# Kernel tuning notes

Hardware: AMD Instinct MI355X
Metric: run time of the kernel (lower is better)

The kernel has to match this reference:

```python
import jax, jax.numpy as jnp
import numpy as np

DIM = 256
DIM_HEAD = 32
HEADS = DIM // DIM_HEAD
SCALE = DIM_HEAD ** -0.5


def setup_inputs() -> dict:
    key = jax.random.key(0)
    ks = jax.random.split(key, 8)
    D1 = DIM + 1
    s = 1.0 / np.sqrt(D1)
    x = jax.random.normal(ks[0], (2, 32, 32, 8, 8, D1), dtype=jnp.float32)
    Wqv = jax.random.normal(ks[1], (D1, DIM), dtype=jnp.float32) * s
    Wkv = jax.random.normal(ks[2], (D1, DIM), dtype=jnp.float32) * s
    Wvv = jax.random.normal(ks[3], (D1, DIM), dtype=jnp.float32) * s
    Wqd = jax.random.normal(ks[4], (D1, 1), dtype=jnp.float32) * s
    Wkd = jax.random.normal(ks[5], (D1, 1), dtype=jnp.float32) * s
    Wvd = jax.random.normal(ks[6], (D1, 1), dtype=jnp.float32) * s
    Wout = jax.random.normal(ks[7], (D1, D1), dtype=jnp.float32) * s
    return {"x": x, "Wqv": Wqv, "Wkv": Wkv, "Wvv": Wvv,
            "Wqd": Wqd, "Wkd": Wkd, "Wvd": Wvd, "Wout": Wout}


def reference(x, Wqv, Wkv, Wvv, Wqd, Wkd, Wvd, Wout):
    b, gx, gy, w1, w2, D1 = x.shape
    B = b * gx * gy          # number of windows
    n = w1 * w2              # tokens per window
    h, dh = HEADS, DIM_HEAD
    xf = x.reshape(B, n, D1)

    def split_heads(t, nh, d):
        # (B, n, nh*d) -> (B, nh, n, d)
        return t.reshape(B, n, nh, d).transpose(0, 2, 1, 3)

    qv = split_heads(xf @ Wqv, h, dh) * SCALE
    kv = split_heads(xf @ Wkv, h, dh)
    vv = split_heads(xf @ Wvv, h, dh)
    qd = split_heads(xf @ Wqd, 1, 1) * SCALE
    kd = split_heads(xf @ Wkd, 1, 1)
    vd = split_heads(xf @ Wvd, 1, 1)

    sim_v = jnp.einsum('bhid,bhjd->bhij', qv, kv)          # (B, h, n, n)
    sim_d = jnp.einsum('bhid,bhjd->bhij', qd, kd)          # (B, 1, n, n)
    sim_m = sim_v * jax.nn.sigmoid(sim_d)                  # depth-gated scores

    attn_v = jax.nn.softmax(sim_m, axis=-1)                # (B, h, n, n)
    attn_d = jax.nn.softmax(jnp.sum(sim_m, axis=1, keepdims=True), axis=-1)  # (B,1,n,n)

    out_v = jnp.einsum('bhij,bhjd->bhid', attn_v, vv)      # (B, h, n, dh)
    out_d = jnp.einsum('bhij,bhjd->bhid', attn_d, vd)      # (B, 1, n, 1)

    out_v = out_v.transpose(0, 2, 1, 3).reshape(B, n, h * dh)  # (B, n, dim)
    out_d = out_d.transpose(0, 2, 1, 3).reshape(B, n, 1)       # (B, n, 1)

    out = jnp.concatenate([out_v, out_d], axis=-1) @ Wout      # (B, n, dim+1)
    return out.reshape(b, gx, gy, w1, w2, D1)
```

## Files before the change

kernel.cpp:

```cpp
#include <hip/hip_runtime.h>


#define D1    257
#define NTOK  64
#define NH    8
#define KT    9
#define NT_CAT 49
#define NT_OUT 17
#define SCALE 0.17677669529663687f

#define XS_OFF    0
#define XS_STRIDE 296
#define OC_STRIDE 288
#define QS_OFF    37888
#define QK_STRIDE 264
#define KS_OFF    71680
#define VS_OFF    105472
#define VS_STRIDE 72
#define AT_OFF    142336
#define AT_STRIDE 72
#define QD_OFF    151552
#define KD_OFF    151808
#define VD_OFF    152064
#define LDS_SIZE  152320

#define WCAT_ELEMS (KT * NT_CAT * 512)
#define WOUT_ELEMS (KT * NT_OUT * 512)

using bf16x8 = __attribute__((ext_vector_type(8))) short;
using s16x4  = __attribute__((ext_vector_type(4))) short;
using f32x4  = __attribute__((ext_vector_type(4))) float;

__device__ __forceinline__ short f2b(float f) {
  unsigned u = __float_as_uint(f);
  u = (u + 0x7FFFu + ((u >> 16) & 1u)) >> 16;
  return (short)u;
}

__device__ __forceinline__ f32x4 mfma16(bf16x8 a, bf16x8 b, f32x4 c) {
  return __builtin_amdgcn_mfma_f32_16x16x32_bf16(a, b, c, 0, 0, 0);
}

__global__ void prep_weights(const float* __restrict__ Wqv, const float* __restrict__ Wkv,
                             const float* __restrict__ Wvv, const float* __restrict__ Wqd,
                             const float* __restrict__ Wkd, const float* __restrict__ Wvd,
                             const float* __restrict__ Wout,
                             short* __restrict__ wcatp, short* __restrict__ woutp) {
  int idx = blockIdx.x * 256 + threadIdx.x;
  if (idx < WCAT_ELEMS) {
    int j = idx & 7, lane = (idx >> 3) & 63, rest = idx >> 9;
    int nt = rest % NT_CAT, kt = rest / NT_CAT;
    int k = 32 * kt + (lane >> 4) * 8 + j;
    int n = 16 * nt + (lane & 15);
    float v = 0.f;
    if (k < D1) {
      if (n < 256)       v = Wqv[k * 256 + n] * SCALE;
      else if (n < 512)  v = Wkv[k * 256 + (n - 256)];
      else if (n < 768)  v = Wvv[k * 256 + (n - 512)];
      else if (n == 768) v = Wqd[k] * SCALE;
      else if (n == 769) v = Wkd[k];
      else if (n == 770) v = Wvd[k];
    }
    wcatp[idx] = f2b(v);
  } else {
    int i2 = idx - WCAT_ELEMS;
    int j = i2 & 7, lane = (i2 >> 3) & 63, rest = i2 >> 9;
    int nt = rest % NT_OUT, kt = rest / NT_OUT;
    int k = 32 * kt + (lane >> 4) * 8 + j;
    int n = 16 * nt + (lane & 15);
    float v = (k < D1 && n < D1) ? Wout[k * D1 + n] : 0.f;
    woutp[i2] = f2b(v);
  }
}

__global__ __launch_bounds__(256, 1)
void vda_attn(const float* __restrict__ x, const short* __restrict__ wcatp,
              const short* __restrict__ woutp, float* __restrict__ out) {
  extern __shared__ char smem[];
  short* xs  = (short*)(smem + XS_OFF);
  short* qs  = (short*)(smem + QS_OFF);
  short* ks  = (short*)(smem + KS_OFF);
  short* vs  = (short*)(smem + VS_OFF);
  short* at  = (short*)(smem + AT_OFF);
  float* qd_s = (float*)(smem + QD_OFF);
  float* kd_s = (float*)(smem + KD_OFF);
  float* vd_s = (float*)(smem + VD_OFF);
  short* oc = xs;

  const int tid  = threadIdx.x;
  const int lane = tid & 63;
  const int w    = tid >> 6;
  const int m    = lane & 15;
  const int q    = lane >> 4;
  const int q8   = q * 8;
  const int win  = blockIdx.x;

  for (int i = tid; i < 64 * 40; i += 256) {
    int r = i / 40, c = 256 + (i % 40);
    if (c > 256) xs[r * XS_STRIDE + c] = 0;
  }
  {
    const float4* xw4 = (const float4*)(x + (size_t)win * (NTOK * D1));
    for (int it = 0; it < 17; ++it) {
      int f4 = tid + it * 256;
      if (f4 < 4112) {
        float4 v = xw4[f4];
        float vals[4] = {v.x, v.y, v.z, v.w};
        int o0 = f4 * 4;
#pragma unroll
        for (int jj = 0; jj < 4; ++jj) {
          int o = o0 + jj;
          int r = o / D1;
          int c = o - r * D1;
          xs[r * XS_STRIDE + c] = f2b(vals[jj]);
        }
      }
    }
  }
  __syncthreads();

  {
    bf16x8 af[4][KT];
#pragma unroll
    for (int mt = 0; mt < 4; ++mt)
#pragma unroll
      for (int kt = 0; kt < KT; ++kt)
        af[mt][kt] = *(const bf16x8*)&xs[(16 * mt + m) * XS_STRIDE + 32 * kt + q8];

    for (int nt = w; nt < NT_CAT; nt += 4) {
      f32x4 acc[4];
#pragma unroll
      for (int mt = 0; mt < 4; ++mt) acc[mt] = f32x4{0.f, 0.f, 0.f, 0.f};
      const short* wp = wcatp + ((size_t)nt * 64 + lane) * 8;
#pragma unroll
      for (int kt = 0; kt < KT; ++kt) {
        bf16x8 bfr = *(const bf16x8*)(wp + (size_t)kt * (NT_CAT * 512));
#pragma unroll
        for (int mt = 0; mt < 4; ++mt)
          acc[mt] = mfma16(af[mt][kt], bfr, acc[mt]);
      }
      int c = nt * 16 + m;
      if (c < 256) {
#pragma unroll
        for (int mt = 0; mt < 4; ++mt)
#pragma unroll
          for (int r = 0; r < 4; ++r)
            qs[(16 * mt + 4 * q + r) * QK_STRIDE + c] = f2b(acc[mt][r]);
      } else if (c < 512) {
#pragma unroll
        for (int mt = 0; mt < 4; ++mt)
#pragma unroll
          for (int r = 0; r < 4; ++r)
            ks[(16 * mt + 4 * q + r) * QK_STRIDE + (c - 256)] = f2b(acc[mt][r]);
      } else if (c < 768) {
        int d = c - 512;
#pragma unroll
        for (int mt = 0; mt < 4; ++mt) {
          s16x4 pk;
#pragma unroll
          for (int r = 0; r < 4; ++r) pk[r] = f2b(acc[mt][r]);
          *(s16x4*)&vs[d * VS_STRIDE + 16 * mt + 4 * q] = pk;
        }
      } else {
        if (m < 3) {
          float* dst = (m == 0) ? qd_s : (m == 1) ? kd_s : vd_s;
#pragma unroll
          for (int mt = 0; mt < 4; ++mt)
#pragma unroll
            for (int r = 0; r < 4; ++r)
              dst[16 * mt + 4 * q + r] = acc[mt][r];
        }
      }
    }
  }
  __syncthreads();

  {
    int row = 16 * w + m;
#pragma unroll
    for (int i = 0; i < 8; ++i)
      oc[row * OC_STRIDE + 256 + q8 + i] = 0;
  }

  float gate[4][4];
  float ssum[4][4];
  {
    float qd_r[4], kd_c[4];
#pragma unroll
    for (int r = 0; r < 4; ++r) qd_r[r] = qd_s[16 * w + 4 * q + r];
#pragma unroll
    for (int nt = 0; nt < 4; ++nt) kd_c[nt] = kd_s[16 * nt + m];
#pragma unroll
    for (int nt = 0; nt < 4; ++nt)
#pragma unroll
      for (int r = 0; r < 4; ++r) {
        float t = qd_r[r] * kd_c[nt];
        gate[nt][r] = 1.f / (1.f + __expf(-t));
        ssum[nt][r] = 0.f;
      }
  }

  short* atw = at + w * (16 * AT_STRIDE);

  for (int h = 0; h < NH; ++h) {
    bf16x8 aq = *(const bf16x8*)&qs[(16 * w + m) * QK_STRIDE + 32 * h + q8];
    f32x4 sv[4];
#pragma unroll
    for (int nt = 0; nt < 4; ++nt) {
      bf16x8 bk = *(const bf16x8*)&ks[(16 * nt + m) * QK_STRIDE + 32 * h + q8];
      f32x4 z = {0.f, 0.f, 0.f, 0.f};
      sv[nt] = mfma16(aq, bk, z);
    }
    float sm[4][4], mx[4], sum[4];
#pragma unroll
    for (int r = 0; r < 4; ++r) mx[r] = -3.4e38f;
#pragma unroll
    for (int nt = 0; nt < 4; ++nt)
#pragma unroll
      for (int r = 0; r < 4; ++r) {
        float s = sv[nt][r] * gate[nt][r];
        ssum[nt][r] += s;
        sm[nt][r] = s;
        mx[r] = fmaxf(mx[r], s);
      }
#pragma unroll
    for (int r = 0; r < 4; ++r) {
#pragma unroll
      for (int msk = 1; msk < 16; msk <<= 1)
        mx[r] = fmaxf(mx[r], __shfl_xor(mx[r], msk));
      sum[r] = 0.f;
    }
#pragma unroll
    for (int nt = 0; nt < 4; ++nt)
#pragma unroll
      for (int r = 0; r < 4; ++r) {
        float p = __expf(sm[nt][r] - mx[r]);
        sm[nt][r] = p;
        sum[r] += p;
      }
#pragma unroll
    for (int r = 0; r < 4; ++r) {
#pragma unroll
      for (int msk = 1; msk < 16; msk <<= 1)
        sum[r] += __shfl_xor(sum[r], msk);
      sum[r] = 1.f / sum[r];
    }
#pragma unroll
    for (int nt = 0; nt < 4; ++nt)
#pragma unroll
      for (int r = 0; r < 4; ++r)
        atw[(4 * q + r) * AT_STRIDE + 16 * nt + m] = f2b(sm[nt][r] * sum[r]);

    bf16x8 a0 = *(const bf16x8*)&atw[m * AT_STRIDE + q8];
    bf16x8 a1 = *(const bf16x8*)&atw[m * AT_STRIDE + 32 + q8];
#pragma unroll
    for (int ntp = 0; ntp < 2; ++ntp) {
      int drow = 32 * h + 16 * ntp + m;
      bf16x8 bv0 = *(const bf16x8*)&vs[drow * VS_STRIDE + q8];
      bf16x8 bv1 = *(const bf16x8*)&vs[drow * VS_STRIDE + 32 + q8];
      f32x4 o = {0.f, 0.f, 0.f, 0.f};
      o = mfma16(a0, bv0, o);
      o = mfma16(a1, bv1, o);
#pragma unroll
      for (int r = 0; r < 4; ++r)
        oc[(16 * w + 4 * q + r) * OC_STRIDE + 32 * h + 16 * ntp + m] = f2b(o[r]);
    }
  }

  {
    float mx[4], sum[4], pd[4][4];
#pragma unroll
    for (int r = 0; r < 4; ++r) mx[r] = -3.4e38f;
#pragma unroll
    for (int nt = 0; nt < 4; ++nt)
#pragma unroll
      for (int r = 0; r < 4; ++r) mx[r] = fmaxf(mx[r], ssum[nt][r]);
#pragma unroll
    for (int r = 0; r < 4; ++r) {
#pragma unroll
      for (int msk = 1; msk < 16; msk <<= 1)
        mx[r] = fmaxf(mx[r], __shfl_xor(mx[r], msk));
      sum[r] = 0.f;
    }
#pragma unroll
    for (int nt = 0; nt < 4; ++nt)
#pragma unroll
      for (int r = 0; r < 4; ++r) {
        pd[nt][r] = __expf(ssum[nt][r] - mx[r]);
        sum[r] += pd[nt][r];
      }
#pragma unroll
    for (int r = 0; r < 4; ++r) {
#pragma unroll
      for (int msk = 1; msk < 16; msk <<= 1)
        sum[r] += __shfl_xor(sum[r], msk);
      sum[r] = 1.f / sum[r];
    }
    float vd_c[4];
#pragma unroll
    for (int nt = 0; nt < 4; ++nt) vd_c[nt] = vd_s[16 * nt + m];
    float ov[4] = {0.f, 0.f, 0.f, 0.f};
#pragma unroll
    for (int nt = 0; nt < 4; ++nt)
#pragma unroll
      for (int r = 0; r < 4; ++r) ov[r] += pd[nt][r] * vd_c[nt];
#pragma unroll
    for (int r = 0; r < 4; ++r) {
#pragma unroll
      for (int msk = 1; msk < 16; msk <<= 1)
        ov[r] += __shfl_xor(ov[r], msk);
    }
    if (m == 0) {
#pragma unroll
      for (int r = 0; r < 4; ++r)
        oc[(16 * w + 4 * q + r) * OC_STRIDE + 256] = f2b(ov[r] * sum[r]);
    }
  }
  __syncthreads();

  for (int nt = w; nt < NT_OUT; nt += 4) {
    f32x4 acc[4];
#pragma unroll
    for (int mt = 0; mt < 4; ++mt) acc[mt] = f32x4{0.f, 0.f, 0.f, 0.f};
#pragma unroll
    for (int kt = 0; kt < KT; ++kt) {
      bf16x8 bw = *(const bf16x8*)(woutp + ((size_t)(kt * NT_OUT + nt) * 64 + lane) * 8);
#pragma unroll
      for (int mt = 0; mt < 4; ++mt) {
        bf16x8 ao = *(const bf16x8*)&oc[(16 * mt + m) * OC_STRIDE + 32 * kt + q8];
        acc[mt] = mfma16(ao, bw, acc[mt]);
      }
    }
    int n = 16 * nt + m;
    if (n < D1) {
#pragma unroll
      for (int mt = 0; mt < 4; ++mt)
#pragma unroll
        for (int r = 0; r < 4; ++r)
          out[((size_t)win * NTOK + 16 * mt + 4 * q + r) * D1 + n] = acc[mt][r];
    }
  }
}

extern "C" void kernel_launch(void* const* d_in, const int* in_sizes, int n_in,
                              void* d_out, int out_size, void* d_ws, size_t ws_size,
                              hipStream_t stream) {
  (void)n_in; (void)out_size; (void)ws_size;
  const float* x    = (const float*)d_in[0];
  const float* Wqv  = (const float*)d_in[1];
  const float* Wkv  = (const float*)d_in[2];
  const float* Wvv  = (const float*)d_in[3];
  const float* Wqd  = (const float*)d_in[4];
  const float* Wkd  = (const float*)d_in[5];
  const float* Wvd  = (const float*)d_in[6];
  const float* Wout = (const float*)d_in[7];
  float* out = (float*)d_out;

  short* wcatp = (short*)d_ws;
  short* woutp = wcatp + WCAT_ELEMS;

  int nwin = in_sizes[0] / (NTOK * D1);

  hipFuncSetAttribute((const void*)vda_attn, hipFuncAttributeMaxDynamicSharedMemorySize, LDS_SIZE);

  int prep_blocks = (WCAT_ELEMS + WOUT_ELEMS) / 256;
  prep_weights<<<prep_blocks, 256, 0, stream>>>(Wqv, Wkv, Wvv, Wqd, Wkd, Wvd, Wout, wcatp, woutp);
  vda_attn<<<nwin, 256, LDS_SIZE, stream>>>(x, wcatp, woutp, out);
}
```

Measured before the change: 582.2 us.

## Use 1024-thread blocks splitting heads across waves with LDS atomics for depth sum

Raises each window's block from 4 to 16 waves. The QKV projection and output GEMM now spread N-tiles across 16 waves. The attention phase gives each wave a row tile and a head pair, and the per-head score sums for the depth softmax are combined through LDS atomicAdds. V is stored pre-swizzled in MFMA fragment order so it can be read contiguously, and the attention scratch reuses the Q region. The aim is to hide latency with more waves per CU now that LDS allows only one block, at the cost of extra barriers, more register pressure under 1024-thread launch bounds, and atomic traffic.

```diff
diff --git a/kernel.cpp b/kernel.cpp
--- a/kernel.cpp
+++ b/kernel.cpp
@@ -11,18 +11,18 @@
 
 #define XS_OFF    0
 #define XS_STRIDE 296
-#define OC_STRIDE 288
+#define OC_STRIDE 296
 #define QS_OFF    37888
 #define QK_STRIDE 264
-#define KS_OFF    71680
-#define VS_OFF    105472
-#define VS_STRIDE 72
-#define AT_OFF    142336
-#define AT_STRIDE 72
-#define QD_OFF    151552
-#define KD_OFF    151808
-#define VD_OFF    152064
-#define LDS_SIZE  152320
+#define AT_STRIDE 68
+#define KS_OFF    72704
+#define VS_OFF    106496
+#define DS_OFF    139264
+#define DS_STRIDE 65
+#define QD_OFF    155904
+#define KD_OFF    156160
+#define VD_OFF    156416
+#define LDS_SIZE  156672
 
 #define WCAT_ELEMS (KT * NT_CAT * 512)
 #define WOUT_ELEMS (KT * NT_OUT * 512)
@@ -73,7 +73,7 @@
   }
 }
 
-__global__ __launch_bounds__(256, 1)
+__global__ __launch_bounds__(1024)
 void vda_attn(const float* __restrict__ x, const short* __restrict__ wcatp,
               const short* __restrict__ woutp, float* __restrict__ out) {
   extern __shared__ char smem[];
@@ -81,7 +81,7 @@
   short* qs  = (short*)(smem + QS_OFF);
   short* ks  = (short*)(smem + KS_OFF);
   short* vs  = (short*)(smem + VS_OFF);
-  short* at  = (short*)(smem + AT_OFF);
+  float* dsum = (float*)(smem + DS_OFF);
   float* qd_s = (float*)(smem + QD_OFF);
   float* kd_s = (float*)(smem + KD_OFF);
   float* vd_s = (float*)(smem + VD_OFF);
@@ -95,71 +95,78 @@
   const int q8   = q * 8;
   const int win  = blockIdx.x;
 
-  for (int i = tid; i < 64 * 40; i += 256) {
-    int r = i / 40, c = 256 + (i % 40);
-    if (c > 256) xs[r * XS_STRIDE + c] = 0;
-  }
+  for (int i = tid; i < 64 * 39; i += 1024) {
+    int r = i / 39, c = 257 + (i % 39);
+    xs[r * XS_STRIDE + c] = 0;
+  }
+  for (int i = tid; i < 64 * DS_STRIDE; i += 1024) dsum[i] = 0.f;
   {
     const float4* xw4 = (const float4*)(x + (size_t)win * (NTOK * D1));
-    for (int it = 0; it < 17; ++it) {
-      int f4 = tid + it * 256;
-      if (f4 < 4112) {
-        float4 v = xw4[f4];
-        float vals[4] = {v.x, v.y, v.z, v.w};
-        int o0 = f4 * 4;
-#pragma unroll
-        for (int jj = 0; jj < 4; ++jj) {
-          int o = o0 + jj;
-          int r = o / D1;
-          int c = o - r * D1;
-          xs[r * XS_STRIDE + c] = f2b(vals[jj]);
+    for (int f4 = tid; f4 < 4112; f4 += 1024) {
+      float4 v = xw4[f4];
+      float vals[4] = {v.x, v.y, v.z, v.w};
+      int o0 = f4 * 4;
+      int r0 = o0 / D1, c0 = o0 - r0 * D1;
+#pragma unroll
+      for (int jj = 0; jj < 4; ++jj) {
+        int c = c0 + jj, r = r0;
+        if (c >= D1) { c -= D1; r += 1; }
+        xs[r * XS_STRIDE + c] = f2b(vals[jj]);
+      }
+    }
+  }
+  __syncthreads();
+
+  {
+    f32x4 acc[4][4];
+#pragma unroll
+    for (int t = 0; t < 4; ++t)
+#pragma unroll
+      for (int mt = 0; mt < 4; ++mt) acc[t][mt] = f32x4{0.f, 0.f, 0.f, 0.f};
+
+    for (int kt = 0; kt < KT; ++kt) {
+      bf16x8 af[4];
+#pragma unroll
+      for (int mt = 0; mt < 4; ++mt)
+        af[mt] = *(const bf16x8*)&xs[(16 * mt + m) * XS_STRIDE + 32 * kt + q8];
+#pragma unroll
+      for (int t = 0; t < 4; ++t) {
+        int nt = w + 16 * t;
+        if (nt < NT_CAT) {
+          bf16x8 bfr = *(const bf16x8*)(wcatp + ((size_t)(kt * NT_CAT + nt) * 64 + lane) * 8);
+#pragma unroll
+          for (int mt = 0; mt < 4; ++mt)
+            acc[t][mt] = mfma16(af[mt], bfr, acc[t][mt]);
         }
       }
     }
-  }
-  __syncthreads();
-
-  {
-    bf16x8 af[4][KT];
-#pragma unroll
-    for (int mt = 0; mt < 4; ++mt)
-#pragma unroll
-      for (int kt = 0; kt < KT; ++kt)
-        af[mt][kt] = *(const bf16x8*)&xs[(16 * mt + m) * XS_STRIDE + 32 * kt + q8];
-
-    for (int nt = w; nt < NT_CAT; nt += 4) {
-      f32x4 acc[4];
-#pragma unroll
-      for (int mt = 0; mt < 4; ++mt) acc[mt] = f32x4{0.f, 0.f, 0.f, 0.f};
-      const short* wp = wcatp + ((size_t)nt * 64 + lane) * 8;
-#pragma unroll
-      for (int kt = 0; kt < KT; ++kt) {
-        bf16x8 bfr = *(const bf16x8*)(wp + (size_t)kt * (NT_CAT * 512));
-#pragma unroll
-        for (int mt = 0; mt < 4; ++mt)
-          acc[mt] = mfma16(af[mt][kt], bfr, acc[mt]);
-      }
+#pragma unroll
+    for (int t = 0; t < 4; ++t) {
+      int nt = w + 16 * t;
+      if (nt >= NT_CAT) continue;
       int c = nt * 16 + m;
       if (c < 256) {
 #pragma unroll
         for (int mt = 0; mt < 4; ++mt)
 #pragma unroll
           for (int r = 0; r < 4; ++r)
-            qs[(16 * mt + 4 * q + r) * QK_STRIDE + c] = f2b(acc[mt][r]);
+            qs[(16 * mt + 4 * q + r) * QK_STRIDE + c] = f2b(acc[t][mt][r]);
       } else if (c < 512) {
 #pragma unroll
         for (int mt = 0; mt < 4; ++mt)
 #pragma unroll
           for (int r = 0; r < 4; ++r)
-            ks[(16 * mt + 4 * q + r) * QK_STRIDE + (c - 256)] = f2b(acc[mt][r]);
+            ks[(16 * mt + 4 * q + r) * QK_STRIDE + (c - 256)] = f2b(acc[t][mt][r]);
       } else if (c < 768) {
-        int d = c - 512;
 #pragma unroll
         for (int mt = 0; mt < 4; ++mt) {
+          int frag = (nt - 32) * 2 + (mt >> 1);
+          int q2 = (2 * mt + (q >> 1)) & 3;
+          int j0 = 4 * (q & 1);
           s16x4 pk;
 #pragma unroll
-          for (int r = 0; r < 4; ++r) pk[r] = f2b(acc[mt][r]);
-          *(s16x4*)&vs[d * VS_STRIDE + 16 * mt + 4 * q] = pk;
+          for (int r = 0; r < 4; ++r) pk[r] = f2b(acc[t][mt][r]);
+          *(s16x4*)&vs[frag * 512 + (q2 * 16 + m) * 8 + j0] = pk;
         }
       } else {
         if (m < 3) {
@@ -168,26 +175,26 @@
           for (int mt = 0; mt < 4; ++mt)
 #pragma unroll
             for (int r = 0; r < 4; ++r)
-              dst[16 * mt + 4 * q + r] = acc[mt][r];
+              dst[16 * mt + 4 * q + r] = acc[t][mt][r];
         }
       }
     }
   }
   __syncthreads();
 
-  {
-    int row = 16 * w + m;
-#pragma unroll
-    for (int i = 0; i < 8; ++i)
-      oc[row * OC_STRIDE + 256 + q8 + i] = 0;
-  }
-
-  float gate[4][4];
-  float ssum[4][4];
+  const int rw = w & 3;
+  const int hp = w >> 2;
+
+  bf16x8 aq[2];
+#pragma unroll
+  for (int hh = 0; hh < 2; ++hh)
+    aq[hh] = *(const bf16x8*)&qs[(16 * rw + m) * QK_STRIDE + 32 * (2 * hp + hh) + q8];
+
+  float gate[4][4], ssum[4][4];
   {
     float qd_r[4], kd_c[4];
 #pragma unroll
-    for (int r = 0; r < 4; ++r) qd_r[r] = qd_s[16 * w + 4 * q + r];
+    for (int r = 0; r < 4; ++r) qd_r[r] = qd_s[16 * rw + 4 * q + r];
 #pragma unroll
     for (int nt = 0; nt < 4; ++nt) kd_c[nt] = kd_s[16 * nt + m];
 #pragma unroll
@@ -199,17 +206,24 @@
         ssum[nt][r] = 0.f;
       }
   }
-
-  short* atw = at + w * (16 * AT_STRIDE);
-
-  for (int h = 0; h < NH; ++h) {
-    bf16x8 aq = *(const bf16x8*)&qs[(16 * w + m) * QK_STRIDE + 32 * h + q8];
+  __syncthreads();
+
+  if (hp == 0) {
+    bf16x8 z = {0, 0, 0, 0, 0, 0, 0, 0};
+    *(bf16x8*)&oc[(16 * rw + m) * OC_STRIDE + 256 + q8] = z;
+  }
+
+  short* atw = (short*)(smem + QS_OFF) + w * (16 * AT_STRIDE);
+
+#pragma unroll
+  for (int hh = 0; hh < 2; ++hh) {
+    int h = 2 * hp + hh;
     f32x4 sv[4];
 #pragma unroll
     for (int nt = 0; nt < 4; ++nt) {
       bf16x8 bk = *(const bf16x8*)&ks[(16 * nt + m) * QK_STRIDE + 32 * h + q8];
       f32x4 z = {0.f, 0.f, 0.f, 0.f};
-      sv[nt] = mfma16(aq, bk, z);
+      sv[nt] = mfma16(aq[hh], bk, z);
     }
     float sm[4][4], mx[4], sum[4];
 #pragma unroll
@@ -251,30 +265,47 @@
       for (int r = 0; r < 4; ++r)
         atw[(4 * q + r) * AT_STRIDE + 16 * nt + m] = f2b(sm[nt][r] * sum[r]);
 
-    bf16x8 a0 = *(const bf16x8*)&atw[m * AT_STRIDE + q8];
-    bf16x8 a1 = *(const bf16x8*)&atw[m * AT_STRIDE + 32 + q8];
+    s16x4 l0 = *(const s16x4*)&atw[m * AT_STRIDE + q8];
+    s16x4 l1 = *(const s16x4*)&atw[m * AT_STRIDE + q8 + 4];
+    s16x4 l2 = *(const s16x4*)&atw[m * AT_STRIDE + 32 + q8];
+    s16x4 l3 = *(const s16x4*)&atw[m * AT_STRIDE + 32 + q8 + 4];
+    bf16x8 a0, a1;
+#pragma unroll
+    for (int j = 0; j < 4; ++j) { a0[j] = l0[j]; a0[4 + j] = l1[j]; a1[j] = l2[j]; a1[4 + j] = l3[j]; }
+
 #pragma unroll
     for (int ntp = 0; ntp < 2; ++ntp) {
-      int drow = 32 * h + 16 * ntp + m;
-      bf16x8 bv0 = *(const bf16x8*)&vs[drow * VS_STRIDE + q8];
-      bf16x8 bv1 = *(const bf16x8*)&vs[drow * VS_STRIDE + 32 + q8];
+      bf16x8 bv0 = *(const bf16x8*)&vs[(((2 * h + ntp) * 2) + 0) * 512 + lane * 8];
+      bf16x8 bv1 = *(const bf16x8*)&vs[(((2 * h + ntp) * 2) + 1) * 512 + lane * 8];
       f32x4 o = {0.f, 0.f, 0.f, 0.f};
       o = mfma16(a0, bv0, o);
       o = mfma16(a1, bv1, o);
 #pragma unroll
       for (int r = 0; r < 4; ++r)
-        oc[(16 * w + 4 * q + r) * OC_STRIDE + 32 * h + 16 * ntp + m] = f2b(o[r]);
-    }
-  }
-
-  {
-    float mx[4], sum[4], pd[4][4];
+        oc[(16 * rw + 4 * q + r) * OC_STRIDE + 32 * h + 16 * ntp + m] = f2b(o[r]);
+    }
+  }
+
+#pragma unroll
+  for (int nt = 0; nt < 4; ++nt)
+#pragma unroll
+    for (int r = 0; r < 4; ++r)
+      atomicAdd(&dsum[(16 * rw + 4 * q + r) * DS_STRIDE + 16 * nt + m], ssum[nt][r]);
+  __syncthreads();
+
+  if (hp == 0) {
+    float sd[4][4], mx[4], sum[4];
+#pragma unroll
+    for (int nt = 0; nt < 4; ++nt)
+#pragma unroll
+      for (int r = 0; r < 4; ++r)
+        sd[nt][r] = dsum[(16 * rw + 4 * q + r) * DS_STRIDE + 16 * nt + m];
 #pragma unroll
     for (int r = 0; r < 4; ++r) mx[r] = -3.4e38f;
 #pragma unroll
     for (int nt = 0; nt < 4; ++nt)
 #pragma unroll
-      for (int r = 0; r < 4; ++r) mx[r] = fmaxf(mx[r], ssum[nt][r]);
+      for (int r = 0; r < 4; ++r) mx[r] = fmaxf(mx[r], sd[nt][r]);
 #pragma unroll
     for (int r = 0; r < 4; ++r) {
 #pragma unroll
@@ -286,8 +317,8 @@
     for (int nt = 0; nt < 4; ++nt)
 #pragma unroll
       for (int r = 0; r < 4; ++r) {
-        pd[nt][r] = __expf(ssum[nt][r] - mx[r]);
-        sum[r] += pd[nt][r];
+        sd[nt][r] = __expf(sd[nt][r] - mx[r]);
+        sum[r] += sd[nt][r];
       }
 #pragma unroll
     for (int r = 0; r < 4; ++r) {
@@ -303,7 +334,7 @@
 #pragma unroll
     for (int nt = 0; nt < 4; ++nt)
 #pragma unroll
-      for (int r = 0; r < 4; ++r) ov[r] += pd[nt][r] * vd_c[nt];
+      for (int r = 0; r < 4; ++r) ov[r] += sd[nt][r] * vd_c[nt];
 #pragma unroll
     for (int r = 0; r < 4; ++r) {
 #pragma unroll
@@ -313,31 +344,46 @@
     if (m == 0) {
 #pragma unroll
       for (int r = 0; r < 4; ++r)
-        oc[(16 * w + 4 * q + r) * OC_STRIDE + 256] = f2b(ov[r] * sum[r]);
+        oc[(16 * rw + 4 * q + r) * OC_STRIDE + 256] = f2b(ov[r] * sum[r]);
     }
   }
   __syncthreads();
 
-  for (int nt = w; nt < NT_OUT; nt += 4) {
-    f32x4 acc[4];
-#pragma unroll
-    for (int mt = 0; mt < 4; ++mt) acc[mt] = f32x4{0.f, 0.f, 0.f, 0.f};
-#pragma unroll
+  {
+    f32x4 acc2[2][4];
+#pragma unroll
+    for (int t = 0; t < 2; ++t)
+#pragma unroll
+      for (int mt = 0; mt < 4; ++mt) acc2[t][mt] = f32x4{0.f, 0.f, 0.f, 0.f};
+
     for (int kt = 0; kt < KT; ++kt) {
-      bf16x8 bw = *(const bf16x8*)(woutp + ((size_t)(kt * NT_OUT + nt) * 64 + lane) * 8);
-#pragma unroll
-      for (int mt = 0; mt < 4; ++mt) {
-        bf16x8 ao = *(const bf16x8*)&oc[(16 * mt + m) * OC_STRIDE + 32 * kt + q8];
-        acc[mt] = mfma16(ao, bw, acc[mt]);
-      }
-    }
-    int n = 16 * nt + m;
-    if (n < D1) {
+      bf16x8 ao[4];
 #pragma unroll
       for (int mt = 0; mt < 4; ++mt)
-#pragma unroll
-        for (int r = 0; r < 4; ++r)
-          out[((size_t)win * NTOK + 16 * mt + 4 * q + r) * D1 + n] = acc[mt][r];
+        ao[mt] = *(const bf16x8*)&oc[(16 * mt + m) * OC_STRIDE + 32 * kt + q8];
+#pragma unroll
+      for (int t = 0; t < 2; ++t) {
+        int nt = w + 16 * t;
+        if (nt < NT_OUT) {
+          bf16x8 bw = *(const bf16x8*)(woutp + ((size_t)(kt * NT_OUT + nt) * 64 + lane) * 8);
+#pragma unroll
+          for (int mt = 0; mt < 4; ++mt)
+            acc2[t][mt] = mfma16(ao[mt], bw, acc2[t][mt]);
+        }
+      }
+    }
+#pragma unroll
+    for (int t = 0; t < 2; ++t) {
+      int nt = w + 16 * t;
+      if (nt >= NT_OUT) continue;
+      int n = 16 * nt + m;
+      if (n < D1) {
+#pragma unroll
+        for (int mt = 0; mt < 4; ++mt)
+#pragma unroll
+          for (int r = 0; r < 4; ++r)
+            out[((size_t)win * NTOK + 16 * mt + 4 * q + r) * D1 + n] = acc2[t][mt][r];
+      }
     }
   }
 }
@@ -365,5 +411,5 @@
 
   int prep_blocks = (WCAT_ELEMS + WOUT_ELEMS) / 256;
   prep_weights<<<prep_blocks, 256, 0, stream>>>(Wqv, Wkv, Wvv, Wqd, Wkd, Wvd, Wout, wcatp, woutp);
-  vda_attn<<<nwin, 256, LDS_SIZE, stream>>>(x, wcatp, woutp, out);
+  vda_attn<<<nwin, 1024, LDS_SIZE, stream>>>(x, wcatp, woutp, out);
 }
```

Result: faster. 563.1 us (-3.3%).
